# Optimization experiments

Hardware: AMD Instinct MI355X
Metric: run time of the kernel (lower is better)

## Reference

```python
import jax, jax.numpy as jnp
import numpy as np

K = 20
EPS = 1e-5


def _knn_idx(x, k):
    # x: [B, N, D] -> indices of k nearest neighbors per node (self included,
    # matching torch_cluster.knn(x, x, k)).
    sq = jnp.sum(x * x, axis=-1)                      # [B, N]
    d = sq[:, :, None] + sq[:, None, :] - 2.0 * jnp.einsum('bnd,bmd->bnm', x, x)
    return jax.lax.top_k(-d, k)[1]                    # [B, N, k]


def _edge_feat(x, idx):
    # EdgeConv edge feature: concat(x_i, x_j - x_i)  -> [B, N, k, 2D]
    xj = jax.vmap(lambda xb, ib: xb[ib])(x, idx)      # [B, N, k, D]
    xi = jnp.broadcast_to(x[:, :, None, :], xj.shape)
    return jnp.concatenate([xi, xj - xi], axis=-1)


def _bn(h, g, b):
    # training-mode batch norm over all edges (PyG MLP default norm)
    mean = jnp.mean(h, axis=(0, 1, 2), keepdims=True)
    var = jnp.var(h, axis=(0, 1, 2), keepdims=True)
    return g * (h - mean) * jax.lax.rsqrt(var + EPS) + b


def _lin_init(key, fin, fout):
    k1, k2 = jax.random.split(key)
    s = 1.0 / np.sqrt(fin)
    W = jax.random.uniform(k1, (fin, fout), jnp.float32, -s, s)
    b = jax.random.uniform(k2, (fout,), jnp.float32, -s, s)
    return W, b


def setup_inputs() -> dict:
    key = jax.random.key(0)
    ks = jax.random.split(key, 8)
    B, N = 32, 1024
    pos = jax.random.normal(ks[0], (B, N, 3), jnp.float32)
    W1, b1 = _lin_init(ks[1], 6, 64)
    W2, b2 = _lin_init(ks[2], 64, 64)
    W3, b3 = _lin_init(ks[3], 64, 64)
    Wc2, bc2 = _lin_init(ks[4], 128, 128)
    Wl, bl = _lin_init(ks[5], 192, 1024)
    Wm1, bm1 = _lin_init(ks[6], 1024, 512)
    Wm2, bm2 = _lin_init(ks[7], 512, 256)
    Wm3, bm3 = _lin_init(jax.random.fold_in(key, 99), 256, 40)
    g1 = jnp.ones((64,), jnp.float32); be1 = jnp.zeros((64,), jnp.float32)
    g2 = jnp.ones((64,), jnp.float32); be2 = jnp.zeros((64,), jnp.float32)
    return dict(pos=pos, W1=W1, b1=b1, g1=g1, be1=be1, W2=W2, b2=b2, g2=g2,
                be2=be2, W3=W3, b3=b3, Wc2=Wc2, bc2=bc2, Wl=Wl, bl=bl,
                Wm1=Wm1, bm1=bm1, Wm2=Wm2, bm2=bm2, Wm3=Wm3, bm3=bm3)


def reference(pos, W1, b1, g1, be1, W2, b2, g2, be2, W3, b3, Wc2, bc2,
              Wl, bl, Wm1, bm1, Wm2, bm2, Wm3, bm3):
    # DynamicEdgeConv 1: kNN in coordinate space, MLP [6,64,64,64] (plain last)
    e1 = _edge_feat(pos, _knn_idx(pos, K))            # [B, N, k, 6]
    h = jax.nn.relu(_bn(e1 @ W1 + b1, g1, be1))
    h = jax.nn.relu(_bn(h @ W2 + b2, g2, be2))
    h = h @ W3 + b3
    x1 = jnp.max(h, axis=2)                           # [B, N, 64] max aggr
    # DynamicEdgeConv 2: kNN in feature space, single plain Linear 128->128
    e2 = _edge_feat(x1, _knn_idx(x1, K))              # [B, N, k, 128]
    x2 = jnp.max(e2 @ Wc2 + bc2, axis=2)              # [B, N, 128]
    # linear + global max pool + head MLP (norm=None, dropout=identity/eval)
    lin = jnp.concatenate([x1, x2], axis=-1) @ Wl + bl  # [B, N, 1024]
    pooled = jnp.max(lin, axis=1)                     # [B, 1024]
    h = jax.nn.relu(pooled @ Wm1 + bm1)
    h = jax.nn.relu(h @ Wm2 + bm2)
    return h @ Wm3 + bm3                              # [B, 40]
```

## Files before the change

### kernel.cpp

```cpp
#include <hip/hip_runtime.h>
#include <hip/hip_bf16.h>
#include <float.h>
#include <math.h>

typedef __hip_bfloat16 bf16;
typedef unsigned long long u64;

#define BATCH 32
#define NPTS  1024
#define KNN   20
#define NB    (BATCH*NPTS)
#define NEDGE (NB*KNN)

#define OFF_FLAG 512u
#define OFF_INB  1024u
#define OFF_IDX  988928u
#define OFF_X1   1644288u
#define OFF_X2   3741440u
#define OFF_C1   5838592u
#define OFF_POOL 7935744u
#define SLOW_END 8066816u
#define OFF_B2H  8066816u
#define FAST_END 10163968u
#define IN_POSF 0u
#define IN_B1   98304u
#define IN_G1   98368u
#define IN_BE1  98432u
#define IN_B2   98496u
#define IN_G2   98560u
#define IN_BE2  98624u
#define IN_B3   98688u
#define IN_BC2  98752u
#define IN_BL   98880u
#define IN_BM1  99904u
#define IN_BM2  100416u
#define IN_BM3  100672u
#define IN_W1   100736u
#define IN_WBUF 101120u
#define WB_W2   0u
#define WB_W3   4096u
#define WB_WD   8192u
#define WB_WBOT 16384u
#define WB_WL   24576u
#define WB_WM1  221184u
#define WB_WM2  745472u
#define WB_WM3  876544u
#define IN_TOTAL 987904u

__device__ __forceinline__ float bf2f(bf16 v){ return __bfloat162float(v); }

__device__ __forceinline__ unsigned int mono32(float f){
  unsigned int b = __float_as_uint(f);
  return b ^ ((unsigned int)((int)b >> 31) | 0x80000000u);
}

typedef __attribute__((ext_vector_type(8))) short bf16x8;
typedef __attribute__((ext_vector_type(4))) float f32x4;

__device__ __forceinline__ unsigned short bfhi(float f){
  unsigned int u = __float_as_uint(f);
  u += 0x7FFFu + ((u >> 16) & 1u);
  return (unsigned short)(u >> 16);
}
__device__ __forceinline__ void bfsplit(float f, unsigned short& h, unsigned short& l){
  h = bfhi(f);
  float fh = __uint_as_float(((unsigned int)h) << 16);
  l = bfhi(f - fh);
}

#define REP20(M) M(0) M(1) M(2) M(3) M(4) M(5) M(6) M(7) M(8) M(9) \
                 M(10) M(11) M(12) M(13) M(14) M(15) M(16) M(17) M(18) M(19)
#define SH19(M) M(19,18) M(18,17) M(17,16) M(16,15) M(15,14) M(14,13) M(13,12) \
                M(12,11) M(11,10) M(10,9) M(9,8) M(8,7) M(7,6) M(6,5) M(5,4) \
                M(4,3) M(3,2) M(2,1) M(1,0)

__device__ __forceinline__ double packkey(float d, int idx){
  unsigned int b = __float_as_uint(fmaxf(d, 0.0f));
  u64 k = 0x4000000000000000ULL | ((u64)b << 20) | (unsigned int)idx;
  return __longlong_as_double((long long)k);
}

#define KDECLD(p) double rk##p = DBL_MAX;
#define KMM(p,pm) rk##p = fmin(rk##p, fmax(rk##pm, _k));
#define INS_MM(kv) do{ double _k=(kv); SH19(KMM) rk0 = fmin(rk0, _k); }while(0)

#define KPUB_A(p) mrgA[q_l*21+p] = (u64)__double_as_longlong(rk##p);
#define KPUB_B(p) mrgB[q_l*21+p] = (u64)__double_as_longlong(rk##p);
#define KSTG(p)   gpart[p] = (u64)__double_as_longlong(rk##p);
#define KLDAD(p)  double rk##p = __longlong_as_double((long long)pa[p]);
#define KOUTU(p)  optr[p] = (int)((u64)__double_as_longlong(rk##p) & 1023ULL);

__global__ void k_sniff(const void* pos_raw, int* flag){
  if (blockIdx.x == 0 && threadIdx.x == 0){
    const unsigned short* h = (const unsigned short*)pos_raw;
    int wild = 0;
    for (int k = 0; k < 16; k++){
      unsigned int bits = ((unsigned int)h[2*k]) << 16;
      float v = __uint_as_float(bits);
      float a = fabsf(v);
      if (a != 0.0f && (v != v || a > 1e10f || a < 1e-10f)) wild++;
    }
    *flag = (wild >= 4) ? 1 : 0;
  }
}

__device__ __forceinline__ float rdv(const void* p, int i, int f){
  return f ? ((const float*)p)[i] : bf2f(((const bf16*)p)[i]);
}

__global__ __launch_bounds__(256) void k_cvt(
    const void* pos, const void* W1, const void* b1, const void* g1, const void* be1,
    const void* W2, const void* b2, const void* g2, const void* be2,
    const void* W3, const void* b3, const void* Wc2, const void* bc2,
    const void* Wl, const void* bl, const void* Wm1, const void* bm1,
    const void* Wm2, const void* bm2, const void* Wm3, const void* bm3,
    const int* flag, float* inb){
  int id = blockIdx.x*256 + threadIdx.x;
  if (id >= (int)IN_TOTAL) return;
  int f = *flag;
  float v;
  if      (id < 98304)  v = rdv(pos, id, f);
  else if (id < 98368)  v = rdv(b1,  id-98304, f);
  else if (id < 98432)  v = rdv(g1,  id-98368, f);
  else if (id < 98496)  v = rdv(be1, id-98432, f);
  else if (id < 98560)  v = rdv(b2,  id-98496, f);
  else if (id < 98624)  v = rdv(g2,  id-98560, f);
  else if (id < 98688)  v = rdv(be2, id-98624, f);
  else if (id < 98752)  v = rdv(b3,  id-98688, f);
  else if (id < 98880)  v = rdv(bc2, id-98752, f);
  else if (id < 99904)  v = rdv(bl,  id-98880, f);
  else if (id < 100416) v = rdv(bm1, id-99904, f);
  else if (id < 100672) v = rdv(bm2, id-100416, f);
  else if (id < 100712) v = rdv(bm3, id-100672, f);
  else if (id < 100736) v = 0.0f;
  else if (id < 101120) v = rdv(W1,  id-100736, f);
  else {
    int t = id - 101120;
    if      (t < 4096)   v = rdv(W2, t, f);
    else if (t < 8192)   v = rdv(W3, t-4096, f);
    else if (t < 16384){ int u = t-8192;  v = rdv(Wc2, u, f) - rdv(Wc2, 8192+u, f); }
    else if (t < 24576){ int u = t-16384; v = rdv(Wc2, 8192+u, f); }
    else if (t < 221184) v = rdv(Wl,  t-24576, f);
    else if (t < 745472){ int u = t-221184; int c = u>>10, d = u&1023; v = rdv(Wm1, d*512+c, f); }
    else if (t < 876544){ int u = t-745472; int c = u>>9,  d = u&511;  v = rdv(Wm2, d*256+c, f); }
    else               { int u = t-876544; int c = u>>8,  d = u&255;  v = rdv(Wm3, d*40+c, f); }
  }
  inb[id] = v;
}

__global__ __launch_bounds__(256) void k_prep1(const float* inb, float* a1, float* c1){
  const float* posf = inb + IN_POSF;
  const float* W1f  = inb + IN_W1;
  const float* b1f  = inb + IN_B1;
  int id = blockIdx.x*256 + threadIdx.x;
  int bn = id >> 6, c = id & 63;
  float p0 = posf[bn*3], p1 = posf[bn*3+1], p2 = posf[bn*3+2];
  float wt0 = W1f[c],     wt1 = W1f[64+c],  wt2 = W1f[128+c];
  float wb0 = W1f[192+c], wb1 = W1f[256+c], wb2 = W1f[320+c];
  float cv = p0*wb0 + p1*wb1 + p2*wb2;
  float av = p0*(wt0-wb0) + p1*(wt1-wb1) + p2*(wt2-wb2) + b1f[c];
  a1[id] = av;  c1[id] = cv;
}

__global__ __launch_bounds__(256, 2) void k_knn1(const float* inb, u64* part){
  const float* posf = inb + IN_POSF;
  __shared__ __align__(16) char sm1[21504];
  float* psx = (float*)sm1;
  float* psy = psx + 1024;
  float* psz = psy + 1024;
  float* sqs = psz + 1024;
  u64* mrgA = (u64*)sm1;
  u64* mrgB = (u64*)(sm1 + 10752);
  int bb   = blockIdx.x >> 5;
  int qg   = (blockIdx.x >> 1) & 15;
  int half = blockIdx.x & 1;
  int tid = threadIdx.x;
  int q_l = tid & 63;
  int slot = tid >> 6;
  for (int t = tid; t < 1024; t += 256){
    float x = posf[(bb*1024+t)*3], y = posf[(bb*1024+t)*3+1], z = posf[(bb*1024+t)*3+2];
    psx[t] = x; psy[t] = y; psz[t] = z; sqs[t] = x*x + y*y + z*z;
  }
  __syncthreads();
  int i_l = qg*64 + q_l;
  float xi0 = psx[i_l], xi1 = psy[i_l], xi2 = psz[i_l];
  float sqi = sqs[i_l];
  REP20(KDECLD)
  int cbase = half*512;
  for (int u = 0; u < 128; u++){
    int jj = cbase + 4*u + slot;
    float dot = xi0*psx[jj] + xi1*psy[jj] + xi2*psz[jj];
    float d = sqi + sqs[jj] - 2.0f*dot;
    INS_MM(packkey(d, jj));
  }
  __syncthreads();
  if (slot == 1){ REP20(KPUB_A) }
  if (slot == 3){ REP20(KPUB_B) }
  __syncthreads();
  if ((slot & 1) == 0){
    const u64* src = (slot == 0) ? &mrgA[q_l*21] : &mrgB[q_l*21];
    for (int p = 0; p < KNN; p++){
      double kv = __longlong_as_double((long long)src[p]);
      if (kv > rk19) break;
      INS_MM(kv);
    }
  }
  __syncthreads();
  if (slot == 2){ REP20(KPUB_B) }
  __syncthreads();
  if (slot == 0){
    const u64* src = &mrgB[q_l*21];
    for (int p = 0; p < KNN; p++){
      double kv = __longlong_as_double((long long)src[p]);
      if (kv > rk19) break;
      INS_MM(kv);
    }
    int gi = bb*1024 + i_l;
    u64* gpart = part + ((size_t)gi*2 + half)*KNN;
    REP20(KSTG)
  }
}

__global__ __launch_bounds__(256) void k_mrg(const u64* part, int* out){
  int gi = blockIdx.x*256 + threadIdx.x;
  const u64* pa = part + (size_t)gi*2*KNN;
  REP20(KLDAD)
  for (int p = 0; p < KNN; p++){
    double kv = __longlong_as_double((long long)pa[KNN + p]);
    if (kv > rk19) break;
    INS_MM(kv);
  }
  int* optr = out + gi*KNN;
  REP20(KOUTU)
}

__global__ __launch_bounds__(256) void k_stats1(const float* a1, const float* c1,
                                                const int* idx1, double* stats){
  __shared__ float rs[256], rs2[256];
  int tid = threadIdx.x, c = tid & 63, slot = tid >> 6;
  int base = blockIdx.x * 1024;
  float s = 0.f, s2 = 0.f;
  for (int t = 0; t < 256; t++){
    unsigned e = (unsigned)(base + t*4 + slot);
    int i = (int)(e / 20u);
    int b = i >> 10;
    int j = idx1[e];
    float h = a1[i*64+c] + c1[((b<<10)+j)*64 + c];
    s += h; s2 += h*h;
  }
  rs[tid] = s; rs2[tid] = s2;
  __syncthreads();
  if (slot == 0){
    double ts  = (double)rs[c]  + (double)rs[64+c]  + (double)rs[128+c]  + (double)rs[192+c];
    double ts2 = (double)rs2[c] + (double)rs2[64+c] + (double)rs2[128+c] + (double)rs2[192+c];
    atomicAdd(&stats[c], ts);
    atomicAdd(&stats[64+c], ts2);
  }
}


__global__ __launch_bounds__(256) void k_stats2m(const float* a1, const float* c1,
    const int* idx1, const float* inb, double* stats){
  __shared__ __align__(16) unsigned short W2hF[4096], W2lF[4096];
  __shared__ float sc1s[64], sh1s[64];
  __shared__ float rs[4][64], rs2[4][64];
  int tid = threadIdx.x;
  const float* wbuf = inb + IN_WBUF;
  for (int t = tid; t < 4096; t += 256){
    int nt = t >> 10, ks = (t >> 9) & 1, ln = (t >> 3) & 63, e = t & 7;
    int row = ks*32 + (ln >> 4)*8 + e;
    int col = nt*16 + (ln & 15);
    unsigned short hh, ll;
    bfsplit(wbuf[WB_W2 + row*64 + col], hh, ll);
    W2hF[t] = hh; W2lF[t] = ll;
  }
  if (tid < 64){
    int c = tid;
    const double M = (double)NEDGE;
    double m1 = stats[c]/M;
    double v1 = stats[64+c]/M - m1*m1;
    double r1 = 1.0/sqrt(v1 + 1e-5);
    double g1 = (double)inb[IN_G1 + c];
    sc1s[c] = (float)(g1*r1);
    sh1s[c] = (float)((double)inb[IN_BE1 + c] - m1*g1*r1);
  }
  __syncthreads();
  int lane = tid & 63, wv = tid >> 6;
  int c16 = lane & 15, ag = lane >> 4, kb0 = ag*8;
  float sa[4] = {0,0,0,0}, qa[4] = {0,0,0,0};
  for (int rd = 0; rd < 3; rd++){
    int T = rd*4 + wv;
    if (T < 10){
      int krow = 16*T + c16;
      int node = (krow*52429) >> 20;
      int nodeg = blockIdx.x*8 + node;
      int j = idx1[blockIdx.x*160 + krow];
      int gj = ((nodeg >> 10) << 10) + j;
      const float* ar = a1 + (size_t)nodeg*64;
      const float* cr = c1 + (size_t)gj*64;
      f32x4 av0 = *(const f32x4*)(ar + kb0);
      f32x4 av1 = *(const f32x4*)(ar + kb0 + 4);
      f32x4 av2 = *(const f32x4*)(ar + 32 + kb0);
      f32x4 av3 = *(const f32x4*)(ar + 36 + kb0);
      f32x4 cv0 = *(const f32x4*)(cr + kb0);
      f32x4 cv1 = *(const f32x4*)(cr + kb0 + 4);
      f32x4 cv2 = *(const f32x4*)(cr + 32 + kb0);
      f32x4 cv3 = *(const f32x4*)(cr + 36 + kb0);
      bf16x8 a0h, a0l, a1h_, a1l_;
      #pragma unroll
      for (int e = 0; e < 4; e++){
        unsigned short hh, ll;
        float h;
        h = fmaxf((av0[e]+cv0[e])*sc1s[kb0+e] + sh1s[kb0+e], 0.f);
        bfsplit(h, hh, ll); a0h[e] = (short)hh; a0l[e] = (short)ll;
        h = fmaxf((av1[e]+cv1[e])*sc1s[kb0+4+e] + sh1s[kb0+4+e], 0.f);
        bfsplit(h, hh, ll); a0h[4+e] = (short)hh; a0l[4+e] = (short)ll;
// ... 127 lines not shown
      f32x4 pacc[4];
      #pragma unroll
      for (int nt = 0; nt < 4; nt++){
        bf16x8 wh0 = *(const bf16x8*)(W2hF + (nt*2+0)*512 + lane*8);
        bf16x8 wh1 = *(const bf16x8*)(W2hF + (nt*2+1)*512 + lane*8);
        bf16x8 wl0 = *(const bf16x8*)(W2lF + (nt*2+0)*512 + lane*8);
        bf16x8 wl1 = *(const bf16x8*)(W2lF + (nt*2+1)*512 + lane*8);
        f32x4 acc = {0.f, 0.f, 0.f, 0.f};
        acc = __builtin_amdgcn_mfma_f32_16x16x32_bf16(a0h,  wh0, acc, 0, 0, 0);
        acc = __builtin_amdgcn_mfma_f32_16x16x32_bf16(a1h_, wh1, acc, 0, 0, 0);
        acc = __builtin_amdgcn_mfma_f32_16x16x32_bf16(a0h,  wl0, acc, 0, 0, 0);
        acc = __builtin_amdgcn_mfma_f32_16x16x32_bf16(a1h_, wl1, acc, 0, 0, 0);
        acc = __builtin_amdgcn_mfma_f32_16x16x32_bf16(a0l,  wh0, acc, 0, 0, 0);
        acc = __builtin_amdgcn_mfma_f32_16x16x32_bf16(a1l_, wh1, acc, 0, 0, 0);
        pacc[nt] = acc;
      }
      #pragma unroll
      for (int nt = 0; nt < 4; nt++){
        #pragma unroll
        for (int r = 0; r < 4; r++){
          float v = fmaxf(pacc[nt][r]*scn[nt] + shn[nt], 0.f);
          sw[(4*ag + r)*68 + nt*16 + c16] = v;
        }
      }
      f32x4 h20 = *(const f32x4*)(sw + c16*68 + kb0);
      f32x4 h21 = *(const f32x4*)(sw + c16*68 + kb0 + 4);
      f32x4 h22 = *(const f32x4*)(sw + c16*68 + 32 + kb0);
      f32x4 h23 = *(const f32x4*)(sw + c16*68 + 36 + kb0);
      bf16x8 b0h, b0l, b1h, b1l;
      #pragma unroll
      for (int e = 0; e < 4; e++){
        unsigned short hh, ll;
        bfsplit(h20[e], hh, ll); b0h[e] = (short)hh; b0l[e] = (short)ll;
        bfsplit(h21[e], hh, ll); b0h[4+e] = (short)hh; b0l[4+e] = (short)ll;
        bfsplit(h22[e], hh, ll); b1h[e] = (short)hh; b1l[e] = (short)ll;
        bfsplit(h23[e], hh, ll); b1h[4+e] = (short)hh; b1l[4+e] = (short)ll;
      }
      int rowA = 16*T;
      int nA = (rowA*52429) >> 20;
      int bnd = nA*20 + 20 - rowA;
      int hasB = (bnd < 16);
      #pragma unroll
      for (int nt = 0; nt < 4; nt++){
        bf16x8 wh0 = *(const bf16x8*)(W3hF + (nt*2+0)*512 + lane*8);
        bf16x8 wh1 = *(const bf16x8*)(W3hF + (nt*2+1)*512 + lane*8);
        bf16x8 wl0 = *(const bf16x8*)(W3lF + (nt*2+0)*512 + lane*8);
        bf16x8 wl1 = *(const bf16x8*)(W3lF + (nt*2+1)*512 + lane*8);
        f32x4 acc = {0.f, 0.f, 0.f, 0.f};
        acc = __builtin_amdgcn_mfma_f32_16x16x32_bf16(b0h, wh0, acc, 0, 0, 0);
        acc = __builtin_amdgcn_mfma_f32_16x16x32_bf16(b1h, wh1, acc, 0, 0, 0);
        acc = __builtin_amdgcn_mfma_f32_16x16x32_bf16(b0h, wl0, acc, 0, 0, 0);
        acc = __builtin_amdgcn_mfma_f32_16x16x32_bf16(b1h, wl1, acc, 0, 0, 0);
        acc = __builtin_amdgcn_mfma_f32_16x16x32_bf16(b0l, wh0, acc, 0, 0, 0);
        acc = __builtin_amdgcn_mfma_f32_16x16x32_bf16(b1l, wh1, acc, 0, 0, 0);
        float mA = -FLT_MAX, mB = -FLT_MAX;
        #pragma unroll
        for (int r = 0; r < 4; r++){
          int rw = 4*ag + r;
          float v = acc[r];
          bool inA = (rw < bnd);
          mA = inA ? fmaxf(mA, v) : mA;
          mB = inA ? mB : fmaxf(mB, v);
        }
        mA = fmaxf(mA, __shfl_xor(mA, 16));
        mA = fmaxf(mA, __shfl_xor(mA, 32));
        mB = fmaxf(mB, __shfl_xor(mB, 16));
        mB = fmaxf(mB, __shfl_xor(mB, 32));
        if (ag == 0){
          atomicMax(&mxp2[nA][nt*16 + c16], mono32(mA));
          if (hasB) atomicMax(&mxp2[nA+1][nt*16 + c16], mono32(mB));
        }
      }
    }
  }
  __syncthreads();
  for (int s = tid; s < 512; s += 256){
    int nl = s >> 6, c = s & 63;
    unsigned int u = mxp2[nl][c];
    unsigned int bts = (u & 0x80000000u) ? (u ^ 0x80000000u) : ~u;
    x1[(size_t)(blockIdx.x*8 + nl)*64 + c] = __uint_as_float(bts) + inb[IN_B3 + c];
  }
}

__global__ __launch_bounds__(256, 4) void k_knn2(const float* x1, u64* part){
  __shared__ __align__(16) char sm2[35584];
  unsigned short* Ch = (unsigned short*)sm2;
  unsigned short* Cl = (unsigned short*)(sm2 + 9216);
  float* Dd  = (float*)(sm2 + 18432);
  float* sqc = (float*)(sm2 + 35072);
  float* sqq = (float*)(sm2 + 35328);
  u64* mrgA = (u64*)sm2;
  u64* mrgB = (u64*)(sm2 + 10752);
  int bb   = blockIdx.x >> 5;
  int qg   = (blockIdx.x >> 1) & 15;
  int half = blockIdx.x & 1;
  int tid = threadIdx.x;
  int q_l = tid & 63;
  int wv = tid >> 6;
  int lane = tid & 63;
  int c16 = lane & 15, ag = lane >> 4, kb0 = ag*8;
  int qbase = bb*1024 + qg*64;
  bf16x8 qh0, qh1, ql0, ql1;
  {
    const float* qr = x1 + (size_t)(qbase + wv*16 + c16)*64;
    f32x4 v0 = *(const f32x4*)(qr + kb0);
    f32x4 v1 = *(const f32x4*)(qr + kb0 + 4);
    f32x4 v2 = *(const f32x4*)(qr + 32 + kb0);
    f32x4 v3 = *(const f32x4*)(qr + 36 + kb0);
    #pragma unroll
    for (int e = 0; e < 4; e++){
      unsigned short hh, ll;
      bfsplit(v0[e], hh, ll); qh0[e] = (short)hh; ql0[e] = (short)ll;
      bfsplit(v1[e], hh, ll); qh0[4+e] = (short)hh; ql0[4+e] = (short)ll;
      bfsplit(v2[e], hh, ll); qh1[e] = (short)hh; ql1[e] = (short)ll;
      bfsplit(v3[e], hh, ll); qh1[4+e] = (short)hh; ql1[4+e] = (short)ll;
    }
  }
  if (tid < 64){
    const float* xr = x1 + (size_t)(qbase + tid)*64;
    float s = 0.f;
    #pragma unroll
    for (int d4 = 0; d4 < 16; d4++){
      f32x4 v = *(const f32x4*)(xr + d4*4);
      s += v[0]*v[0] + v[1]*v[1] + v[2]*v[2] + v[3]*v[3];
    }
    sqq[tid] = s;
  }
  REP20(KDECLD)
  for (int ch = 0; ch < 8; ch++){
    int c0 = half*512 + ch*64;
    __syncthreads();
    for (int pp = tid; pp < 2048; pp += 256){
      int row = pp >> 5, cp = pp & 31;
      const float* src = x1 + (size_t)(bb*1024 + c0 + row)*64 + cp*2;
      float v0 = src[0], v1 = src[1];
      unsigned short h0, l0, h1, l1;
      bfsplit(v0, h0, l0); bfsplit(v1, h1, l1);
      ((unsigned int*)Ch)[row*36 + cp] = (unsigned int)h0 | ((unsigned int)h1 << 16);
      ((unsigned int*)Cl)[row*36 + cp] = (unsigned int)l0 | ((unsigned int)l1 << 16);
    }
    __syncthreads();
    if (tid < 64){
      float s = 0.f;
      for (int dw = 0; dw < 32; dw++){
        unsigned int hw = ((unsigned int*)Ch)[tid*36 + dw];
        unsigned int lw = ((unsigned int*)Cl)[tid*36 + dw];
        float a0 = __uint_as_float(hw << 16) + __uint_as_float(lw << 16);
        float a1 = __uint_as_float(hw & 0xFFFF0000u) + __uint_as_float(lw & 0xFFFF0000u);
        s += a0*a0 + a1*a1;
      }
      sqc[tid] = s;
    }
    __syncthreads();
    #pragma unroll
    for (int nt = 0; nt < 4; nt++){
      bf16x8 bh0 = *(const bf16x8*)(Ch + (nt*16 + c16)*72 + kb0);
      bf16x8 bh1 = *(const bf16x8*)(Ch + (nt*16 + c16)*72 + 32 + kb0);
      bf16x8 bl0 = *(const bf16x8*)(Cl + (nt*16 + c16)*72 + kb0);
      bf16x8 bl1 = *(const bf16x8*)(Cl + (nt*16 + c16)*72 + 32 + kb0);
      f32x4 p0 = {0.f,0.f,0.f,0.f}, p1 = {0.f,0.f,0.f,0.f}, p2 = {0.f,0.f,0.f,0.f};
      p0 = __builtin_amdgcn_mfma_f32_16x16x32_bf16(qh0, bh0, p0, 0, 0, 0);
      p0 = __builtin_amdgcn_mfma_f32_16x16x32_bf16(qh1, bh1, p0, 0, 0, 0);
      p1 = __builtin_amdgcn_mfma_f32_16x16x32_bf16(qh0, bl0, p1, 0, 0, 0);
      p1 = __builtin_amdgcn_mfma_f32_16x16x32_bf16(qh1, bl1, p1, 0, 0, 0);
      p2 = __builtin_amdgcn_mfma_f32_16x16x32_bf16(ql0, bh0, p2, 0, 0, 0);
      p2 = __builtin_amdgcn_mfma_f32_16x16x32_bf16(ql1, bh1, p2, 0, 0, 0);
      #pragma unroll
      for (int r = 0; r < 4; r++){
        int qrow = wv*16 + 4*ag + r;
        float d = sqq[qrow] + sqc[nt*16 + c16] - 2.0f*(p0[r] + p1[r] + p2[r]);
        Dd[qrow*65 + nt*16 + c16] = d;
      }
    }
    __syncthreads();
    for (int u = 0; u < 16; u += 2){
      int cA = 4*u + wv, cB = 4*(u+1) + wv;
      float dA = Dd[q_l*65 + cA];
      float dB = Dd[q_l*65 + cB];
      INS_MM(packkey(dA, c0 + cA));
      INS_MM(packkey(dB, c0 + cB));
    }
  }
  __syncthreads();
  if (wv == 1){ REP20(KPUB_A) }
  if (wv == 3){ REP20(KPUB_B) }
  __syncthreads();
  if ((wv & 1) == 0){
    const u64* src = (wv == 0) ? &mrgA[q_l*21] : &mrgB[q_l*21];
    for (int p = 0; p < KNN; p++){
      double kv = __longlong_as_double((long long)src[p]);
      if (kv > rk19) break;
      INS_MM(kv);
    }
  }
  __syncthreads();
  if (wv == 2){ REP20(KPUB_B) }
  __syncthreads();
  if (wv == 0){
    const u64* src = &mrgB[q_l*21];
    for (int p = 0; p < KNN; p++){
      double kv = __longlong_as_double((long long)src[p]);
      if (kv > rk19) break;
      INS_MM(kv);
    }
    int gi = qbase + q_l;
    u64* gpart = part + ((size_t)gi*2 + half)*KNN;
    REP20(KSTG)
  }
}

__global__ __launch_bounds__(256) void k_B2h(const float* x1, const float* inb,
                                             int q, float* B2H){
  __shared__ __align__(16) float Wbh[4096];
  __shared__ __align__(16) float xsh[1024];
  int tid = threadIdx.x;
  const float* Wb = inb + IN_WBUF + WB_WBOT;
  for (int t = tid; t < 4096; t += 256){
    int r = t >> 6, cl = t & 63;
    Wbh[t] = Wb[r*128 + q*64 + cl];
  }
  int node0 = blockIdx.x * 16;
  for (int t = tid; t < 1024; t += 256) xsh[t] = x1[node0*64 + t];
  __syncthreads();
  int n_l = tid >> 4, cg = tid & 15;
  const float* xr = xsh + n_l*64;
  float4 acc = make_float4(0.f,0.f,0.f,0.f);
  #pragma unroll 8
  for (int d = 0; d < 64; d++){
    float v = xr[d];
    float4 w = *(const float4*)(Wbh + d*64 + cg*4);
    acc.x += v*w.x; acc.y += v*w.y; acc.z += v*w.z; acc.w += v*w.w;
  }
  *(float4*)(B2H + (node0 + n_l)*64 + cg*4) = acc;
}

__global__ __launch_bounds__(256) void k_x2h(const float* x1, const float* B2H,
                                             const float* inb, const int* idx2,
                                             int q, float* x2){
  __shared__ __align__(16) float Wdh[4096];
  __shared__ __align__(16) float xsh[256];
  int tid = threadIdx.x;
  const float* Wd = inb + IN_WBUF + WB_WD;
  for (int t = tid; t < 4096; t += 256){
    int r = t >> 6, cl = t & 63;
    Wdh[t] = Wd[r*128 + q*64 + cl];
  }
  int node0 = blockIdx.x * 4;
  xsh[tid] = x1[node0*64 + tid];
  __syncthreads();
  int n_l = tid >> 6, cl = tid & 63;
  int i = node0 + n_l;
  int b = i >> 10;
  const float* xr = xsh + n_l*64;
  float acc = inb[IN_BC2 + q*64 + cl];
  #pragma unroll 8
  for (int d = 0; d < 64; d++) acc += xr[d]*Wdh[d*64 + cl];
  float m = -FLT_MAX;
  for (int kk = 0; kk < KNN; kk++){
    int j = idx2[i*KNN + kk];
    m = fmaxf(m, B2H[((b<<10)+j)*64 + cl]);
  }
  x2[i*128 + q*64 + cl] = acc + m;
}

__global__ __launch_bounds__(256) void k_x2d(const float* x1, const float* inb,
                                             const int* idx2, float* x2){
  __shared__ __align__(16) float Wdh[4096], Wbh[4096];
  __shared__ __align__(16) float xis[1024], xjs[1024];
  int tid = threadIdx.x;
  int q = blockIdx.x & 1;
  int node0 = (blockIdx.x >> 1) * 16;
  const float* Wd = inb + IN_WBUF + WB_WD;
  const float* Wb = inb + IN_WBUF + WB_WBOT;
  for (int t = tid; t < 4096; t += 256){
    int r = t >> 6, cl = t & 63;
    Wdh[t] = Wd[r*128 + q*64 + cl];
    Wbh[t] = Wb[r*128 + q*64 + cl];
  }
  for (int t = tid; t < 1024; t += 256) xis[t] = x1[node0*64 + t];
  __syncthreads();
  int n_l = tid >> 4, cg = tid & 15;
  int i = node0 + n_l, b = i >> 10;
  const float* xr = xis + n_l*64;
  float4 af = make_float4(inb[IN_BC2 + q*64 + cg*4],   inb[IN_BC2 + q*64 + cg*4+1],
                          inb[IN_BC2 + q*64 + cg*4+2], inb[IN_BC2 + q*64 + cg*4+3]);
  #pragma unroll 8
  for (int d = 0; d < 64; d++){
    float v = xr[d];
    float4 w = *(const float4*)(Wdh + d*64 + cg*4);
    af.x += v*w.x; af.y += v*w.y; af.z += v*w.z; af.w += v*w.w;
// ... 116 lines not shown
  f32x4 p1 = *(const f32x4*)(pl + lane*16 + 4);
  f32x4 p2 = *(const f32x4*)(pl + lane*16 + 8);
  f32x4 p3 = *(const f32x4*)(pl + lane*16 + 12);
  const float* WT = inb + IN_WBUF + WB_WM1;
  #pragma unroll
  for (int cc = 0; cc < 8; cc++){
    int c = cg*32 + wv*8 + cc;
    const float* wr = WT + (size_t)c*1024 + lane*16;
    f32x4 w0 = *(const f32x4*)(wr);
    f32x4 w1 = *(const f32x4*)(wr + 4);
    f32x4 w2 = *(const f32x4*)(wr + 8);
    f32x4 w3 = *(const f32x4*)(wr + 12);
    float acc = w0[0]*p0[0] + w0[1]*p0[1] + w0[2]*p0[2] + w0[3]*p0[3]
              + w1[0]*p1[0] + w1[1]*p1[1] + w1[2]*p1[2] + w1[3]*p1[3]
              + w2[0]*p2[0] + w2[1]*p2[1] + w2[2]*p2[2] + w2[3]*p2[3]
              + w3[0]*p3[0] + w3[1]*p3[1] + w3[2]*p3[2] + w3[3]*p3[3];
    acc += __shfl_xor(acc, 1);  acc += __shfl_xor(acc, 2);
    acc += __shfl_xor(acc, 4);  acc += __shfl_xor(acc, 8);
    acc += __shfl_xor(acc, 16); acc += __shfl_xor(acc, 32);
    if (lane == 0) s1g[b*512 + c] = fmaxf(acc + inb[IN_BM1 + c], 0.f);
  }
}

__global__ __launch_bounds__(256) void k_h2(const float* s1g, const float* inb,
                                            float* s2g){
  __shared__ float s1[512];
  int b = blockIdx.x >> 3, cg = blockIdx.x & 7;
  int tid = threadIdx.x;
  for (int t = tid; t < 512; t += 256) s1[t] = s1g[b*512 + t];
  __syncthreads();
  int wv = tid >> 6, lane = tid & 63;
  f32x4 p0 = *(const f32x4*)(s1 + lane*8);
  f32x4 p1 = *(const f32x4*)(s1 + lane*8 + 4);
  const float* WT = inb + IN_WBUF + WB_WM2;
  #pragma unroll
  for (int cc = 0; cc < 8; cc++){
    int c = cg*32 + wv*8 + cc;
    const float* wr = WT + (size_t)c*512 + lane*8;
    f32x4 w0 = *(const f32x4*)(wr);
    f32x4 w1 = *(const f32x4*)(wr + 4);
    float acc = w0[0]*p0[0] + w0[1]*p0[1] + w0[2]*p0[2] + w0[3]*p0[3]
              + w1[0]*p1[0] + w1[1]*p1[1] + w1[2]*p1[2] + w1[3]*p1[3];
    acc += __shfl_xor(acc, 1);  acc += __shfl_xor(acc, 2);
    acc += __shfl_xor(acc, 4);  acc += __shfl_xor(acc, 8);
    acc += __shfl_xor(acc, 16); acc += __shfl_xor(acc, 32);
    if (lane == 0) s2g[b*256 + c] = fmaxf(acc + inb[IN_BM2 + c], 0.f);
  }
}

__global__ __launch_bounds__(256) void k_h3(const float* s2g, const float* inb,
                                            float* out){
  __shared__ float s2[256];
  int b = blockIdx.x;
  int tid = threadIdx.x;
  s2[tid] = s2g[b*256 + tid];
  __syncthreads();
  int wv = tid >> 6, lane = tid & 63;
  f32x4 p0 = *(const f32x4*)(s2 + lane*4);
  const float* WT = inb + IN_WBUF + WB_WM3;
  for (int cc = 0; cc < 10; cc++){
    int c = wv*10 + cc;
    const float* wr = WT + (size_t)c*256 + lane*4;
    f32x4 w0 = *(const f32x4*)(wr);
    float acc = w0[0]*p0[0] + w0[1]*p0[1] + w0[2]*p0[2] + w0[3]*p0[3];
    acc += __shfl_xor(acc, 1);  acc += __shfl_xor(acc, 2);
    acc += __shfl_xor(acc, 4);  acc += __shfl_xor(acc, 8);
    acc += __shfl_xor(acc, 16); acc += __shfl_xor(acc, 32);
    if (lane == 0) out[b*40 + c] = acc + inb[IN_BM3 + c];
  }
}

extern "C" void kernel_launch(void* const* d_in, const int* in_sizes, int n_in,
                              void* d_out, int out_size, void* d_ws, size_t ws_size,
                              hipStream_t stream){
  float* ws     = (float*)d_ws;
  double* stats = (double*)d_ws;
  int*   flag   = (int*)d_ws + OFF_FLAG;
  float* inb    = ws + OFF_INB;
  int*   idx    = (int*)d_ws + OFF_IDX;
  float* x1p    = ws + OFF_X1;
  float* x2p    = ws + OFF_X2;
  float* a1     = ws + OFF_X2;
  float* c1     = ws + OFF_C1;
  u64*   part   = (u64*)(ws + OFF_X2);
  float* pool4  = ws + OFF_POOL;
  float* B2H    = ws + OFF_B2H;
  float* s1g    = ws + OFF_IDX;
  float* s2g    = ws + OFF_IDX + 16384;
  bool fast = ws_size >= (size_t)FAST_END * 4u;

  hipMemsetAsync(stats, 0, 256*sizeof(double), stream);
  k_sniff<<<1, 64, 0, stream>>>(d_in[0], flag);
  k_cvt<<<3859, 256, 0, stream>>>(
      d_in[0], d_in[1], d_in[2], d_in[3], d_in[4], d_in[5], d_in[6], d_in[7],
      d_in[8], d_in[9], d_in[10], d_in[11], d_in[12], d_in[13], d_in[14],
      d_in[15], d_in[16], d_in[17], d_in[18], d_in[19], d_in[20], flag, inb);
  k_knn1<<<1024, 256, 0, stream>>>(inb, part);
  k_mrg<<<128, 256, 0, stream>>>(part, idx);
  k_prep1<<<8192, 256, 0, stream>>>(inb, a1, c1);
  k_stats1<<<640, 256, 0, stream>>>(a1, c1, idx, stats);
  k_stats2m<<<4096, 256, 0, stream>>>(a1, c1, idx, inb, stats);
  k_x1m<<<4096, 256, 0, stream>>>(a1, c1, idx, inb, stats, x1p);
  k_knn2<<<1024, 256, 0, stream>>>(x1p, part);
  k_mrg<<<128, 256, 0, stream>>>(part, idx);
  if (fast){
    k_B2h<<<2048, 256, 0, stream>>>(x1p, inb, 0, B2H);
    k_x2h<<<8192, 256, 0, stream>>>(x1p, B2H, inb, idx, 0, x2p);
    k_B2h<<<2048, 256, 0, stream>>>(x1p, inb, 1, B2H);
    k_x2h<<<8192, 256, 0, stream>>>(x1p, B2H, inb, idx, 1, x2p);
  } else {
    k_x2d<<<4096, 256, 0, stream>>>(x1p, inb, idx, x2p);
  }
  k_linpoolm<<<512, 512, 0, stream>>>(x1p, x2p, inb, pool4);
  k_h1<<<512, 256, 0, stream>>>(pool4, inb, s1g);
  k_h2<<<256, 256, 0, stream>>>(s1g, inb, s2g);
  k_h3<<<32, 256, 0, stream>>>(s2g, inb, (float*)d_out);
}
```

Before: 762.3 us.

## Two-pass kNN: 32-bit distance threshold, then recompute and collect candidates

Replaces the 64-bit packed (distance,index) top-20 selection with a 32-bit key-only pass that finds the 20th-smallest distance per query. A second kernel recomputes every distance and collects candidates under that threshold (plus slack) with shared atomics, then selects the final 20 with a small serial sort. Using 32-bit min/max instead of double fmin/fmax is meant to make the register insertion network cheaper. The cost is a full second distance pass, including repeating the MFMA dot products for the feature-space kNN, and candidates beyond the 32-slot cap are silently dropped.

```diff
diff --git a/kernel.cpp b/kernel.cpp
--- a/kernel.cpp
+++ b/kernel.cpp
@@ -74,21 +74,39 @@
                 M(12,11) M(11,10) M(10,9) M(9,8) M(8,7) M(7,6) M(6,5) M(5,4) \
                 M(4,3) M(3,2) M(2,1) M(1,0)
 
-__device__ __forceinline__ double packkey(float d, int idx){
-  unsigned int b = __float_as_uint(fmaxf(d, 0.0f));
-  u64 k = 0x4000000000000000ULL | ((u64)b << 20) | (unsigned int)idx;
-  return __longlong_as_double((long long)k);
-}
-
-#define KDECLD(p) double rk##p = DBL_MAX;
-#define KMM(p,pm) rk##p = fmin(rk##p, fmax(rk##pm, _k));
-#define INS_MM(kv) do{ double _k=(kv); SH19(KMM) rk0 = fmin(rk0, _k); }while(0)
-
-#define KPUB_A(p) mrgA[q_l*21+p] = (u64)__double_as_longlong(rk##p);
-#define KPUB_B(p) mrgB[q_l*21+p] = (u64)__double_as_longlong(rk##p);
-#define KSTG(p)   gpart[p] = (u64)__double_as_longlong(rk##p);
-#define KLDAD(p)  double rk##p = __longlong_as_double((long long)pa[p]);
-#define KOUTU(p)  optr[p] = (int)((u64)__double_as_longlong(rk##p) & 1023ULL);
+__device__ __forceinline__ unsigned umin_(unsigned a, unsigned b){ return a<b?a:b; }
+__device__ __forceinline__ unsigned umax_(unsigned a, unsigned b){ return a>b?a:b; }
+
+#define KDECLU(p) unsigned uk##p = 0xFFFFFFFFu;
+#define KMMU(p,pm) uk##p = umin_(uk##p, umax_(uk##pm, _k));
+#define INS_U32(kv) do{ unsigned _k=(kv); SH19(KMMU) uk0 = umin_(uk0, _k); }while(0)
+#define KPUBU_A(p) mrgA[q_l*21+p] = uk##p;
+#define KPUBU_B(p) mrgB[q_l*21+p] = uk##p;
+#define KSTGU(p)   gpart[p] = uk##p;
+#define KLDAU(p)   unsigned uk##p = pa[p];
+
+__device__ __forceinline__ float pdist3(float xi0, float xi1, float xi2, float sqi,
+                                        float px, float py, float pz, float sq){
+  float dot = xi0*px + xi1*py + xi2*pz;
+  return sqi + sq - 2.0f*dot;
+}
+__device__ __forceinline__ float qdist(float sq_q, float sq_c,
+                                       float p0, float p1, float p2){
+  return sq_q + sq_c - 2.0f*(p0 + p1 + p2);
+}
+
+__device__ __forceinline__ void sel20(unsigned* keyr, int* idxr, int n, int* optr){
+  for (int s = 0; s < 20; s++){
+    unsigned bk = 0xFFFFFFFFu; int bi = 0x7FFFFFFF; int bm = 0;
+    for (int t = 0; t < n; t++){
+      unsigned k = keyr[t]; int id = idxr[t];
+      bool better = (k < bk) || (k == bk && id < bi);
+      bk = better ? k : bk; bi = better ? id : bi; bm = better ? t : bm;
+    }
+    optr[s] = (bi == 0x7FFFFFFF) ? 0 : bi;
+    keyr[bm] = 0xFFFFFFFFu; idxr[bm] = 0x7FFFFFFF;
+  }
+}
 
 __global__ void k_sniff(const void* pos_raw, int* flag){
   if (blockIdx.x == 0 && threadIdx.x == 0){
@@ -162,15 +180,15 @@
   a1[id] = av;  c1[id] = cv;
 }
 
-__global__ __launch_bounds__(256, 2) void k_knn1(const float* inb, u64* part){
+__global__ __launch_bounds__(256, 2) void k_knn1a(const float* inb, unsigned* part){
   const float* posf = inb + IN_POSF;
-  __shared__ __align__(16) char sm1[21504];
+  __shared__ __align__(16) char sm1[16384];
   float* psx = (float*)sm1;
   float* psy = psx + 1024;
   float* psz = psy + 1024;
   float* sqs = psz + 1024;
-  u64* mrgA = (u64*)sm1;
-  u64* mrgB = (u64*)(sm1 + 10752);
+  unsigned* mrgA = (unsigned*)sm1;
+  unsigned* mrgB = (unsigned*)(sm1 + 5376);
   int bb   = blockIdx.x >> 5;
   int qg   = (blockIdx.x >> 1) & 15;
   int half = blockIdx.x & 1;
@@ -185,53 +203,89 @@
   int i_l = qg*64 + q_l;
   float xi0 = psx[i_l], xi1 = psy[i_l], xi2 = psz[i_l];
   float sqi = sqs[i_l];
-  REP20(KDECLD)
+  REP20(KDECLU)
   int cbase = half*512;
   for (int u = 0; u < 128; u++){
     int jj = cbase + 4*u + slot;
-    float dot = xi0*psx[jj] + xi1*psy[jj] + xi2*psz[jj];
-    float d = sqi + sqs[jj] - 2.0f*dot;
-    INS_MM(packkey(d, jj));
-  }
-  __syncthreads();
-  if (slot == 1){ REP20(KPUB_A) }
-  if (slot == 3){ REP20(KPUB_B) }
+    float d = pdist3(xi0, xi1, xi2, sqi, psx[jj], psy[jj], psz[jj], sqs[jj]);
+    INS_U32(mono32(d));
+  }
+  __syncthreads();
+  if (slot == 1){ REP20(KPUBU_A) }
+  if (slot == 3){ REP20(KPUBU_B) }
   __syncthreads();
   if ((slot & 1) == 0){
-    const u64* src = (slot == 0) ? &mrgA[q_l*21] : &mrgB[q_l*21];
+    const unsigned* src = (slot == 0) ? &mrgA[q_l*21] : &mrgB[q_l*21];
     for (int p = 0; p < KNN; p++){
-      double kv = __longlong_as_double((long long)src[p]);
-      if (kv > rk19) break;
-      INS_MM(kv);
-    }
-  }
-  __syncthreads();
-  if (slot == 2){ REP20(KPUB_B) }
+      unsigned kv = src[p];
+      if (kv > uk19) break;
+      INS_U32(kv);
+    }
+  }
+  __syncthreads();
+  if (slot == 2){ REP20(KPUBU_B) }
   __syncthreads();
   if (slot == 0){
-    const u64* src = &mrgB[q_l*21];
+    const unsigned* src = &mrgB[q_l*21];
     for (int p = 0; p < KNN; p++){
-      double kv = __longlong_as_double((long long)src[p]);
-      if (kv > rk19) break;
-      INS_MM(kv);
+      unsigned kv = src[p];
+      if (kv > uk19) break;
+      INS_U32(kv);
     }
     int gi = bb*1024 + i_l;
-    u64* gpart = part + ((size_t)gi*2 + half)*KNN;
-    REP20(KSTG)
-  }
-}
-
-__global__ __launch_bounds__(256) void k_mrg(const u64* part, int* out){
+    unsigned* gpart = part + (size_t)(gi*2 + half)*KNN;
+    REP20(KSTGU)
+  }
+}
+
+__global__ __launch_bounds__(256) void k_mrg2(const unsigned* part, unsigned* kthr){
   int gi = blockIdx.x*256 + threadIdx.x;
-  const u64* pa = part + (size_t)gi*2*KNN;
-  REP20(KLDAD)
+  const unsigned* pa = part + (size_t)gi*2*KNN;
+  REP20(KLDAU)
   for (int p = 0; p < KNN; p++){
-    double kv = __longlong_as_double((long long)pa[KNN + p]);
-    if (kv > rk19) break;
-    INS_MM(kv);
-  }
-  int* optr = out + gi*KNN;
-  REP20(KOUTU)
+    unsigned kv = pa[KNN + p];
+    if (kv > uk19) break;
+    INS_U32(kv);
+  }
+  kthr[gi] = uk19;
+}
+
+__global__ __launch_bounds__(256) void k_knn1b(const float* inb, const unsigned* kthr,
+                                               int* idx1){
+  const float* posf = inb + IN_POSF;
+  __shared__ float psx[1024], psy[1024], psz[1024], sqs[1024];
+  __shared__ unsigned cnt[64];
+  __shared__ unsigned keyl[64][33];
+  __shared__ int      idxl[64][33];
+  int bb = blockIdx.x >> 4, qg = blockIdx.x & 15;
+  int tid = threadIdx.x;
+  for (int t = tid; t < 1024; t += 256){
+    float x = posf[(bb*1024+t)*3], y = posf[(bb*1024+t)*3+1], z = posf[(bb*1024+t)*3+2];
+    psx[t] = x; psy[t] = y; psz[t] = z; sqs[t] = x*x + y*y + z*z;
+  }
+  if (tid < 64) cnt[tid] = 0u;
+  __syncthreads();
+  int q_l = tid & 63, slot = tid >> 6;
+  int i_l = qg*64 + q_l;
+  float xi0 = psx[i_l], xi1 = psy[i_l], xi2 = psz[i_l];
+  float sqi = sqs[i_l];
+  unsigned kt = kthr[bb*1024 + i_l];
+  unsigned ktin = kt + 2048u; if (ktin < kt) ktin = 0xFFFFFFFFu;
+  for (int u = 0; u < 256; u++){
+    int jj = 4*u + slot;
+    float d = pdist3(xi0, xi1, xi2, sqi, psx[jj], psy[jj], psz[jj], sqs[jj]);
+    unsigned k = mono32(d);
+    if (k <= ktin){
+      unsigned p = atomicAdd(&cnt[q_l], 1u);
+      if (p < 32u){ keyl[q_l][p] = k; idxl[q_l][p] = jj; }
+    }
+  }
+  __syncthreads();
+  if (tid < 64){
+    int n = (int)umin_(cnt[tid], 32u);
+    int* optr = idx1 + (size_t)(bb*1024 + qg*64 + tid)*KNN;
+    sel20(&keyl[tid][0], &idxl[tid][0], n, optr);
+  }
 }
 
 __global__ __launch_bounds__(256) void k_stats1(const float* a1, const float* c1,
@@ -525,15 +579,15 @@
   }
 }
 
-__global__ __launch_bounds__(256, 4) void k_knn2(const float* x1, u64* part){
+__global__ __launch_bounds__(256, 4) void k_knn2a(const float* x1, unsigned* part){
   __shared__ __align__(16) char sm2[35584];
   unsigned short* Ch = (unsigned short*)sm2;
   unsigned short* Cl = (unsigned short*)(sm2 + 9216);
   float* Dd  = (float*)(sm2 + 18432);
   float* sqc = (float*)(sm2 + 35072);
   float* sqq = (float*)(sm2 + 35328);
-  u64* mrgA = (u64*)sm2;
-  u64* mrgB = (u64*)(sm2 + 10752);
+  unsigned* mrgA = (unsigned*)sm2;
+  unsigned* mrgB = (unsigned*)(sm2 + 5376);
   int bb   = blockIdx.x >> 5;
   int qg   = (blockIdx.x >> 1) & 15;
   int half = blockIdx.x & 1;
@@ -569,7 +623,7 @@
     }
     sqq[tid] = s;
   }
-  REP20(KDECLD)
+  REP20(KDECLU)
   for (int ch = 0; ch < 8; ch++){
     int c0 = half*512 + ch*64;
     __syncthreads();
@@ -611,8 +665,8 @@
       #pragma unroll
       for (int r = 0; r < 4; r++){
         int qrow = wv*16 + 4*ag + r;
-        float d = sqq[qrow] + sqc[nt*16 + c16] - 2.0f*(p0[r] + p1[r] + p2[r]);
-        Dd[qrow*65 + nt*16 + c16] = d;
+        Dd[qrow*65 + nt*16 + c16] =
+            qdist(sqq[qrow], sqc[nt*16 + c16], p0[r], p1[r], p2[r]);
       }
     }
     __syncthreads();
@@ -620,35 +674,145 @@
       int cA = 4*u + wv, cB = 4*(u+1) + wv;
       float dA = Dd[q_l*65 + cA];
       float dB = Dd[q_l*65 + cB];
-      INS_MM(packkey(dA, c0 + cA));
-      INS_MM(packkey(dB, c0 + cB));
-    }
-  }
-  __syncthreads();
-  if (wv == 1){ REP20(KPUB_A) }
-  if (wv == 3){ REP20(KPUB_B) }
+      INS_U32(mono32(dA));
+      INS_U32(mono32(dB));
+    }
+  }
+  __syncthreads();
+  if (wv == 1){ REP20(KPUBU_A) }
+  if (wv == 3){ REP20(KPUBU_B) }
   __syncthreads();
   if ((wv & 1) == 0){
-    const u64* src = (wv == 0) ? &mrgA[q_l*21] : &mrgB[q_l*21];
+    const unsigned* src = (wv == 0) ? &mrgA[q_l*21] : &mrgB[q_l*21];
     for (int p = 0; p < KNN; p++){
-      double kv = __longlong_as_double((long long)src[p]);
-      if (kv > rk19) break;
-      INS_MM(kv);
-    }
-  }
-  __syncthreads();
-  if (wv == 2){ REP20(KPUB_B) }
+      unsigned kv = src[p];
+      if (kv > uk19) break;
+      INS_U32(kv);
+    }
+  }
+  __syncthreads();
+  if (wv == 2){ REP20(KPUBU_B) }
   __syncthreads();
   if (wv == 0){
-    const u64* src = &mrgB[q_l*21];
+    const unsigned* src = &mrgB[q_l*21];
     for (int p = 0; p < KNN; p++){
-      double kv = __longlong_as_double((long long)src[p]);
-      if (kv > rk19) break;
-      INS_MM(kv);
+      unsigned kv = src[p];
+      if (kv > uk19) break;
+      INS_U32(kv);
     }
     int gi = qbase + q_l;
-    u64* gpart = part + ((size_t)gi*2 + half)*KNN;
-    REP20(KSTG)
+    unsigned* gpart = part + (size_t)(gi*2 + half)*KNN;
+    REP20(KSTGU)
+  }
+}
+
+__global__ __launch_bounds__(256) void k_knn2b(const float* x1, const unsigned* kthr,
+                                               int* idx2){
+  __shared__ __align__(16) char sm2[35584];
+  unsigned short* Ch = (unsigned short*)sm2;
+  unsigned short* Cl = (unsigned short*)(sm2 + 9216);
+  float* Dd  = (float*)(sm2 + 18432);
+  float* sqc = (float*)(sm2 + 35072);
+  float* sqq = (float*)(sm2 + 35328);
+  __shared__ unsigned cnt[64];
+  __shared__ unsigned keyl[64][33];
+  __shared__ int      idxl[64][33];
+  int bb = blockIdx.x >> 4, qg = blockIdx.x & 15;
+  int tid = threadIdx.x;
+  int q_l = tid & 63;
+  int wv = tid >> 6;
+  int lane = tid & 63;
+  int c16 = lane & 15, ag = lane >> 4, kb0 = ag*8;
+  int qbase = bb*1024 + qg*64;
+  bf16x8 qh0, qh1, ql0, ql1;
+  {
+    const float* qr = x1 + (size_t)(qbase + wv*16 + c16)*64;
+    f32x4 v0 = *(const f32x4*)(qr + kb0);
+    f32x4 v1 = *(const f32x4*)(qr + kb0 + 4);
+    f32x4 v2 = *(const f32x4*)(qr + 32 + kb0);
+    f32x4 v3 = *(const f32x4*)(qr + 36 + kb0);
+    #pragma unroll
+    for (int e = 0; e < 4; e++){
+      unsigned short hh, ll;
+      bfsplit(v0[e], hh, ll); qh0[e] = (short)hh; ql0[e] = (short)ll;
+      bfsplit(v1[e], hh, ll); qh0[4+e] = (short)hh; ql0[4+e] = (short)ll;
+      bfsplit(v2[e], hh, ll); qh1[e] = (short)hh; ql1[e] = (short)ll;
+      bfsplit(v3[e], hh, ll); qh1[4+e] = (short)hh; ql1[4+e] = (short)ll;
+    }
+  }
+  if (tid < 64){
+    const float* xr = x1 + (size_t)(qbase + tid)*64;
+    float s = 0.f;
+    #pragma unroll
+    for (int d4 = 0; d4 < 16; d4++){
+      f32x4 v = *(const f32x4*)(xr + d4*4);
+      s += v[0]*v[0] + v[1]*v[1] + v[2]*v[2] + v[3]*v[3];
+    }
+    sqq[tid] = s;
+    cnt[tid] = 0u;
+  }
+  unsigned kt = kthr[qbase + q_l];
+  unsigned ktin = kt + 2048u; if (ktin < kt) ktin = 0xFFFFFFFFu;
+  for (int ch = 0; ch < 16; ch++){
+    int c0 = ch*64;
+    __syncthreads();
+    for (int pp = tid; pp < 2048; pp += 256){
+      int row = pp >> 5, cp = pp & 31;
+      const float* src = x1 + (size_t)(bb*1024 + c0 + row)*64 + cp*2;
+      float v0 = src[0], v1 = src[1];
+      unsigned short h0, l0, h1, l1;
+      bfsplit(v0, h0, l0); bfsplit(v1, h1, l1);
+      ((unsigned int*)Ch)[row*36 + cp] = (unsigned int)h0 | ((unsigned int)h1 << 16);
+      ((unsigned int*)Cl)[row*36 + cp] = (unsigned int)l0 | ((unsigned int)l1 << 16);
+    }
+    __syncthreads();
+    if (tid < 64){
+      float s = 0.f;
+      for (int dw = 0; dw < 32; dw++){
+        unsigned int hw = ((unsigned int*)Ch)[tid*36 + dw];
+        unsigned int lw = ((unsigned int*)Cl)[tid*36 + dw];
+        float a0 = __uint_as_float(hw << 16) + __uint_as_float(lw << 16);
+        float a1 = __uint_as_float(hw & 0xFFFF0000u) + __uint_as_float(lw & 0xFFFF0000u);
+        s += a0*a0 + a1*a1;
+      }
+      sqc[tid] = s;
+    }
+    __syncthreads();
+    #pragma unroll
+    for (int nt = 0; nt < 4; nt++){
+      bf16x8 bh0 = *(const bf16x8*)(Ch + (nt*16 + c16)*72 + kb0);
+      bf16x8 bh1 = *(const bf16x8*)(Ch + (nt*16 + c16)*72 + 32 + kb0);
+      bf16x8 bl0 = *(const bf16x8*)(Cl + (nt*16 + c16)*72 + kb0);
+      bf16x8 bl1 = *(const bf16x8*)(Cl + (nt*16 + c16)*72 + 32 + kb0);
+      f32x4 p0 = {0.f,0.f,0.f,0.f}, p1 = {0.f,0.f,0.f,0.f}, p2 = {0.f,0.f,0.f,0.f};
+      p0 = __builtin_amdgcn_mfma_f32_16x16x32_bf16(qh0, bh0, p0, 0, 0, 0);
+      p0 = __builtin_amdgcn_mfma_f32_16x16x32_bf16(qh1, bh1, p0, 0, 0, 0);
+      p1 = __builtin_amdgcn_mfma_f32_16x16x32_bf16(qh0, bl0, p1, 0, 0, 0);
+      p1 = __builtin_amdgcn_mfma_f32_16x16x32_bf16(qh1, bl1, p1, 0, 0, 0);
+      p2 = __builtin_amdgcn_mfma_f32_16x16x32_bf16(ql0, bh0, p2, 0, 0, 0);
+      p2 = __builtin_amdgcn_mfma_f32_16x16x32_bf16(ql1, bh1, p2, 0, 0, 0);
+      #pragma unroll
+      for (int r = 0; r < 4; r++){
+        int qrow = wv*16 + 4*ag + r;
+        Dd[qrow*65 + nt*16 + c16] =
+            qdist(sqq[qrow], sqc[nt*16 + c16], p0[r], p1[r], p2[r]);
+      }
+    }
+    __syncthreads();
+    for (int u = 0; u < 16; u++){
+      int c = 4*u + wv;
+      unsigned k = mono32(Dd[q_l*65 + c]);
+      if (k <= ktin){
+        unsigned p = atomicAdd(&cnt[q_l], 1u);
+        if (p < 32u){ keyl[q_l][p] = k; idxl[q_l][p] = c0 + c; }
+      }
+    }
+  }
+  __syncthreads();
+  if (tid < 64){
+    int n = (int)umin_(cnt[tid], 32u);
+    int* optr = idx2 + (size_t)(qbase + tid)*KNN;
+    sel20(&keyl[tid][0], &idxl[tid][0], n, optr);
   }
 }
 
@@ -931,7 +1095,8 @@
   float* x2p    = ws + OFF_X2;
   float* a1     = ws + OFF_X2;
   float* c1     = ws + OFF_C1;
-  u64*   part   = (u64*)(ws + OFF_X2);
+  unsigned* part32 = (unsigned*)(ws + OFF_X2);
+  unsigned* kthr   = part32 + (size_t)NB*2*KNN;
   float* pool4  = ws + OFF_POOL;
   float* B2H    = ws + OFF_B2H;
   float* s1g    = ws + OFF_IDX;
@@ -944,14 +1109,16 @@
       d_in[0], d_in[1], d_in[2], d_in[3], d_in[4], d_in[5], d_in[6], d_in[7],
       d_in[8], d_in[9], d_in[10], d_in[11], d_in[12], d_in[13], d_in[14],
       d_in[15], d_in[16], d_in[17], d_in[18], d_in[19], d_in[20], flag, inb);
-  k_knn1<<<1024, 256, 0, stream>>>(inb, part);
-  k_mrg<<<128, 256, 0, stream>>>(part, idx);
+  k_knn1a<<<1024, 256, 0, stream>>>(inb, part32);
+  k_mrg2<<<128, 256, 0, stream>>>(part32, kthr);
+  k_knn1b<<<512, 256, 0, stream>>>(inb, kthr, idx);
   k_prep1<<<8192, 256, 0, stream>>>(inb, a1, c1);
   k_stats1<<<640, 256, 0, stream>>>(a1, c1, idx, stats);
   k_stats2m<<<4096, 256, 0, stream>>>(a1, c1, idx, inb, stats);
   k_x1m<<<4096, 256, 0, stream>>>(a1, c1, idx, inb, stats, x1p);
-  k_knn2<<<1024, 256, 0, stream>>>(x1p, part);
-  k_mrg<<<128, 256, 0, stream>>>(part, idx);
+  k_knn2a<<<1024, 256, 0, stream>>>(x1p, part32);
+  k_mrg2<<<128, 256, 0, stream>>>(part32, kthr);
+  k_knn2b<<<512, 256, 0, stream>>>(x1p, kthr, idx);
   if (fast){
     k_B2h<<<2048, 256, 0, stream>>>(x1p, inb, 0, B2H);
     k_x2h<<<8192, 256, 0, stream>>>(x1p, B2H, inb, idx, 0, x2p);
```

Result: slower. 880.5 us (+15.5%).
